# Performance work log

Hardware: AMD Instinct MI355X
Metric: run time of the kernel (lower is better)

The kernel has to match this reference:

```python
import jax, jax.numpy as jnp
import numpy as np

NUM_EXPERTS = 8
INTERM_D = 64  # hardcoded in DynamicConv


def setup_inputs() -> dict:
    key = jax.random.key(0)
    k1, k2, k3, k4 = jax.random.split(key, 4)
    B, C, H, W = 32, 256, 56, 56
    O, K = 256, 3
    x = jax.random.normal(k1, (B, C, H, W), dtype=jnp.float32)
    proj_w = jax.random.normal(k2, (INTERM_D, C), dtype=jnp.float32) * (1.0 / np.sqrt(C))
    proj_b = jax.random.normal(k3, (INTERM_D,), dtype=jnp.float32) * 0.01
    expert_w = jax.random.normal(k4, (NUM_EXPERTS, O, C, K, K), dtype=jnp.float32) * (1.0 / np.sqrt(C * K * K))
    return {"x": x, "proj_w": proj_w, "proj_b": proj_b, "expert_w": expert_w}


def reference(x, proj_w, proj_b, expert_w):
    B, C, H, W = x.shape
    E, O, Cg, K, _ = expert_w.shape
    # --- routing path ---
    pooled = x.mean(axis=(2, 3))                       # [B, C] adaptive_avg_pool2d(.,1)
    rt = pooled @ proj_w.T + proj_b                    # [B, 64]
    r = jax.nn.sigmoid(rt).reshape(B, E, INTERM_D // E).mean(axis=-1)  # avg_pool1d -> [B, E]
    # --- per-sample expert-mixed conv weights ---
    w = jnp.einsum("be,eoikl->boikl", r, expert_w)     # [B, O, C, K, K]
    # --- batched conv via grouped conv (groups = B) ---
    xr = x.reshape(1, B * C, H, W)
    wr = w.reshape(B * O, Cg, K, K)
    out = jax.lax.conv_general_dilated(
        xr, wr,
        window_strides=(1, 1),
        padding=((1, 1), (1, 1)),
        dimension_numbers=("NCHW", "OIHW", "NCHW"),
        feature_group_count=B,
    )                                                   # [1, B*O, H, W]
    return out.reshape(B, O, H, W)
```

## Files before the change

### kernel.cpp

```cpp
#include <hip/hip_runtime.h>
#include <math.h>

typedef unsigned short u16;
typedef __attribute__((ext_vector_type(8))) short    bf16x8;
typedef __attribute__((ext_vector_type(8))) unsigned short u16x8;
typedef __attribute__((ext_vector_type(4))) float    f32x4;

#define NB   32
#define NC   256
#define NO   256
#define NH   56
#define NW   56
#define NP   3136
#define NE   8
#define NID  64
#define HP   58
#define WP   64

#define WMIX_OFF   0
#define XPT_OFF    37748736
#define POOL_OFF   98566144
#define RBUF_OFF   98598912

__device__ __forceinline__ u16 f2bf(float f) {
    unsigned u = __float_as_uint(f);
    unsigned r = (u + 0x7FFFu + ((u >> 16) & 1u)) >> 16;
    return (u16)r;
}

__device__ __forceinline__ void gl_lds16(const void* g, void* l) {
    __builtin_amdgcn_global_load_lds(
        (const __attribute__((address_space(1))) unsigned int*)g,
        (__attribute__((address_space(3))) unsigned int*)l, 16, 0, 0);
}

#define VMCNT0_FENCE() { asm volatile("s_waitcnt vmcnt(0)" ::: "memory"); \
                         __builtin_amdgcn_sched_barrier(0); }

__global__ __launch_bounds__(256) void zero_k(float* __restrict__ pooled,
                                              u16* __restrict__ xpadT) {
    int b = blockIdx.x, t = threadIdx.x;
    pooled[b * 256 + t] = 0.0f;
    u16x8 z = {0, 0, 0, 0, 0, 0, 0, 0};
    u16* r0 = xpadT + ((size_t)(b * HP + 0)) * WP * NC;
    u16* r1 = xpadT + ((size_t)(b * HP + 57)) * WP * NC;
    #pragma unroll
    for (int i = 0; i < 8; ++i) {
        *(u16x8*)&r0[(i * 256 + t) * 8] = z;
        *(u16x8*)&r1[(i * 256 + t) * 8] = z;
    }
}

__global__ __launch_bounds__(256) void transpose_pool_k(const float* __restrict__ x,
                                                        u16* __restrict__ xpadT,
                                                        float* __restrict__ pooled) {
    __shared__ u16 tile[64 * 256];
    int b = blockIdx.x / 56;
    int h = blockIdx.x % 56;
    int t = threadIdx.x;

    int w4 = t & 15, c_sub = t >> 4;
    if (w4 < 14) {
        const float* xp = x + ((size_t)b * NC + c_sub) * NP + (size_t)h * NW + w4 * 4;
        #pragma unroll
        for (int it = 0; it < 16; ++it) {
            int c = it * 16 + c_sub;
            f32x4 v = *(const f32x4*)(xp + (size_t)it * 16 * NP);
            int key = w4;
            int base = ((c >> 3) ^ key) * 8 + (c & 7);
            #pragma unroll
            for (int i = 0; i < 4; ++i)
                tile[(w4 * 4 + i) * 256 + base] = f2bf(v[i]);
        }
    }
    __syncthreads();

    {
        int c8 = t & 31, whi = t >> 5;
        u16* orow = xpadT + ((size_t)(b * HP + h + 1)) * WP * NC;
        #pragma unroll
        for (int j = 0; j < 8; ++j) {
            int wp = whi * 8 + j;
            u16x8 v = {0, 0, 0, 0, 0, 0, 0, 0};
            if (wp >= 1 && wp <= 56) {
                int w = wp - 1;
                v = *(const u16x8*)&tile[w * 256 + ((c8 ^ (w >> 2)) * 8)];
            }
            *(u16x8*)&orow[wp * NC + c8 * 8] = v;
        }
    }

    {
        int c = t;
        int s = c >> 3, sub = c & 7;
        float sum = 0.0f;
        #pragma unroll
        for (int w = 0; w < 56; ++w) {
            u16 u = tile[w * 256 + ((s ^ (w >> 2)) * 8) + sub];
            sum += __uint_as_float(((unsigned)u) << 16);
        }
        atomicAdd(&pooled[b * 256 + c], sum);
    }
}

__global__ __launch_bounds__(64) void routing(const float* __restrict__ pooled,
                                              const float* __restrict__ proj_w,
                                              const float* __restrict__ proj_b,
                                              float* __restrict__ r) {
    __shared__ float ps[256];
    __shared__ float sg[64];
    int b = blockIdx.x, j = threadIdx.x;
    for (int i = j; i < 256; i += 64) ps[i] = pooled[b * NC + i] * (1.0f / 3136.0f);
    __syncthreads();
    float acc = proj_b[j];
    for (int c = 0; c < 256; ++c) acc += ps[c] * proj_w[j * NC + c];
    sg[j] = 1.0f / (1.0f + expf(-acc));
    __syncthreads();
    if (j < NE) {
        float s = 0.0f;
        #pragma unroll
        for (int q = 0; q < 8; ++q) s += sg[j * 8 + q];
        r[b * NE + j] = s * 0.125f;
    }
}

__global__ __launch_bounds__(256) void mix_w(const float* __restrict__ expert_w,
                                             const float* __restrict__ r,
                                             u16* __restrict__ wmix) {
    __shared__ float lr[256];
    int o = blockIdx.x, c = threadIdx.x;
    lr[c] = r[c];
    __syncthreads();
    float w[8][9];
    #pragma unroll
    for (int e = 0; e < 8; ++e) {
        const float* p = expert_w + ((size_t)((e * NO + o) * NC + c)) * 9;
        #pragma unroll
        for (int kk = 0; kk < 9; ++kk) w[e][kk] = p[kk];
    }
    for (int b = 0; b < NB; ++b) {
        float acc[9] = {0, 0, 0, 0, 0, 0, 0, 0, 0};
        #pragma unroll
        for (int e = 0; e < 8; ++e) {
            float rv = lr[b * 8 + e];
            #pragma unroll
            for (int kk = 0; kk < 9; ++kk) acc[kk] += rv * w[e][kk];
        }
        #pragma unroll
        for (int kk = 0; kk < 9; ++kk)
            wmix[((size_t)((b * 9 + kk) * NO + o)) * NC + c] = f2bf(acc[kk]);
    }
}

__global__ __launch_bounds__(256, 2) void conv_k(const u16* __restrict__ wmix,
                                                 const u16* __restrict__ xpadT,
                                                 float* __restrict__ out) {
    __shared__ u16 Bs[256 * 64];
    __shared__ u16 As[2 * 128 * 64];
    char* Bsc = (char*)Bs;
    char* Asc = (char*)As;

    int tid  = threadIdx.x;
    int lane = tid & 63, wid = tid >> 6;
    int ln = lane & 15, hi = lane >> 4;

    int bid = blockIdx.x;
    int logical = (bid & 7) * 224 + (bid >> 3);
    int b   = logical / 56;
    int rem = logical % 56;
    int mt  = rem / 28, nt = rem % 28;
    int obase = mt * 128;
    int h0 = nt * 2;
    int p0 = nt * 112;

    const u16* apane = wmix + (size_t)b * 9 * 65536 + (size_t)obase * 256;
    const u16* xbase = xpadT + ((size_t)(b * HP + h0)) * WP * NC;

    int t3 = tid >> 3, t7 = tid & 7;
    int bstg_src = t3 * 256 + ((t7 ^ (t3 & 7)) * 8);
    int bstg_dst = tid * 16;
    #define STAGE_B(C0) {                                                   \
        _Pragma("unroll")                                                   \
        for (int i = 0; i < 8; ++i)                                         \
            gl_lds16(xbase + (C0) + bstg_src + i * 8192,                    \
                     Bsc + bstg_dst + i * 4096);                            \
    }

    int l3 = lane >> 3, l7 = lane & 7;
    int astg_src = (wid * 32 + l3) * 256 + ((l7 ^ (l3 & 7)) * 8);
    int astg_dst = wid * 4096 + lane * 16;
    #define STAGE_A(KK, C0, BUF) {                                          \
        _Pragma("unroll")                                                   \
        for (int i = 0; i < 4; ++i)                                         \
            gl_lds16(apane + (KK) * 65536 + (C0) + astg_src + i * 2048,     \
                     Asc + (BUF) * 16384 + astg_dst + i * 1024);            \
    }

    f32x4 acc[2][7];
    #pragma unroll
    for (int mi = 0; mi < 2; ++mi)
        #pragma unroll
        for (int ni = 0; ni < 7; ++ni) acc[mi][ni] = (f32x4){0.f, 0.f, 0.f, 0.f};

    int rwbase[7];
    #pragma unroll
    for (int ni = 0; ni < 7; ++ni) {
        int p  = ni * 16 + ln;
        int hr = (p >= 56) ? 1 : 0;
        int wv = p - hr * 56;
        rwbase[ni] = hr * 64 + wv + 1;
    }
    int aoff[2][2];
    #pragma unroll
    for (int mi = 0; mi < 2; ++mi)
        #pragma unroll
        for (int ks = 0; ks < 2; ++ks)
            aoff[mi][ks] = wid * 4096 + (mi * 16 + ln) * 128 +
                           (((ks * 4 + hi) ^ (ln & 7)) << 4);

    STAGE_B(0)
    STAGE_A(0, 0, 0)
    __syncthreads();

    for (int c0 = 0; c0 < 256; c0 += 64) {
        int cc = (c0 >> 6) & 1;
        #pragma unroll
        for (int kk = 0; kk < 9; ++kk) {
            int cur = (cc + kk) & 1;
            if (kk < 8) {
                STAGE_A(kk + 1, c0, cur ^ 1)
            } else if (c0 < 192) {
                STAGE_A(0, c0 + 64, cur ^ 1)
            }
            const int dh = kk / 3, kw = kk % 3;
            const int abase = cur * 16384;
            #pragma unroll
            for (int ks = 0; ks < 2; ++ks) {
                bf16x8 a0 = *(const bf16x8*)(Asc + abase + aoff[0][ks]);
                bf16x8 a1 = *(const bf16x8*)(Asc + abase + aoff[1][ks]);
                #pragma unroll
                for (int ni = 0; ni < 7; ++ni) {
                    int rw   = rwbase[ni] + dh * 64 + kw - 1;
                    int boff = rw * 128 + ((((ks << 2) + hi) ^ (rw & 7)) << 4);
                    bf16x8 bv = *(const bf16x8*)(Bsc + boff);
                    acc[0][ni] = __builtin_amdgcn_mfma_f32_16x16x32_bf16(a0, bv, acc[0][ni], 0, 0, 0);
                    acc[1][ni] = __builtin_amdgcn_mfma_f32_16x16x32_bf16(a1, bv, acc[1][ni], 0, 0, 0);
                }
            }
            VMCNT0_FENCE()
        }
        if (c0 < 192) {
            __syncthreads();
            STAGE_B(c0 + 64)
            __syncthreads();
        }
    }
    #undef STAGE_A
    #undef STAGE_B

    float* op = out + ((size_t)(b * NO + obase + wid * 32)) * NP + p0;
    #pragma unroll
    for (int mi = 0; mi < 2; ++mi)
        #pragma unroll
        for (int ni = 0; ni < 7; ++ni) {
            f32x4 v = acc[mi][ni];
            int col = ni * 16 + ln;
            #pragma unroll
            for (int rg = 0; rg < 4; ++rg) {
                int row = mi * 16 + hi * 4 + rg;
                op[(size_t)row * NP + col] = v[rg];
            }
        }
}

extern "C" void kernel_launch(void* const* d_in, const int* in_sizes, int n_in,
                              void* d_out, int out_size, void* d_ws, size_t ws_size,
                              hipStream_t stream) {
    (void)in_sizes; (void)n_in; (void)out_size; (void)ws_size;
    const float* x        = (const float*)d_in[0];
    const float* proj_w   = (const float*)d_in[1];
    const float* proj_b   = (const float*)d_in[2];
    const float* expert_w = (const float*)d_in[3];
    float* out = (float*)d_out;
    char*  ws  = (char*)d_ws;

    u16*   wmix   = (u16*)(ws + WMIX_OFF);
    u16*   xpadT  = (u16*)(ws + XPT_OFF);
    float* pooled = (float*)(ws + POOL_OFF);
    float* rbuf   = (float*)(ws + RBUF_OFF);

    zero_k<<<dim3(32), dim3(256), 0, stream>>>(pooled, xpadT);
    transpose_pool_k<<<dim3(32 * 56), dim3(256), 0, stream>>>(x, xpadT, pooled);
    routing<<<dim3(32), dim3(64), 0, stream>>>(pooled, proj_w, proj_b, rbuf);
    mix_w<<<dim3(256), dim3(256), 0, stream>>>(expert_w, rbuf, wmix);
    conv_k<<<dim3(32 * 56), dim3(256), 0, stream>>>(wmix, xpadT, out);
}
```

Before: 209.6 us.

## Cover all output channels per block and load weight fragments directly into registers

```diff
diff --git a/kernel.cpp b/kernel.cpp
--- a/kernel.cpp
+++ b/kernel.cpp
@@ -34,9 +34,6 @@
         (__attribute__((address_space(3))) unsigned int*)l, 16, 0, 0);
 }
 
-#define VMCNT0_FENCE() { asm volatile("s_waitcnt vmcnt(0)" ::: "memory"); \
-                         __builtin_amdgcn_sched_barrier(0); }
-
 __global__ __launch_bounds__(256) void zero_k(float* __restrict__ pooled,
                                               u16* __restrict__ xpadT) {
     int b = blockIdx.x, t = threadIdx.x;
@@ -156,25 +153,23 @@
                                                  const u16* __restrict__ xpadT,
                                                  float* __restrict__ out) {
     __shared__ u16 Bs[256 * 64];
-    __shared__ u16 As[2 * 128 * 64];
     char* Bsc = (char*)Bs;
-    char* Asc = (char*)As;
 
     int tid  = threadIdx.x;
     int lane = tid & 63, wid = tid >> 6;
     int ln = lane & 15, hi = lane >> 4;
 
     int bid = blockIdx.x;
-    int logical = (bid & 7) * 224 + (bid >> 3);
-    int b   = logical / 56;
-    int rem = logical % 56;
-    int mt  = rem / 28, nt = rem % 28;
-    int obase = mt * 128;
+    int logical = (bid & 7) * 112 + (bid >> 3);
+    int b  = logical / 28;
+    int nt = logical % 28;
     int h0 = nt * 2;
     int p0 = nt * 112;
 
-    const u16* apane = wmix + (size_t)b * 9 * 65536 + (size_t)obase * 256;
+    const u16* apane = wmix + (size_t)b * 9 * 65536;
     const u16* xbase = xpadT + ((size_t)(b * HP + h0)) * WP * NC;
+
+    const u16* alane = apane + (size_t)(wid * 64 + ln) * 256 + hi * 8;
 
     int t3 = tid >> 3, t7 = tid & 7;
     int bstg_src = t3 * 256 + ((t7 ^ (t3 & 7)) * 8);
@@ -186,19 +181,19 @@
                      Bsc + bstg_dst + i * 4096);                            \
     }
 
-    int l3 = lane >> 3, l7 = lane & 7;
-    int astg_src = (wid * 32 + l3) * 256 + ((l7 ^ (l3 & 7)) * 8);
-    int astg_dst = wid * 4096 + lane * 16;
-    #define STAGE_A(KK, C0, BUF) {                                          \
+    bf16x8 abuf0[8], abuf1[8];
+    #define ISSUE_A(KK, C0, ABUF) {                                         \
+        const u16* ap_ = alane + (KK) * 65536 + (C0);                       \
         _Pragma("unroll")                                                   \
-        for (int i = 0; i < 4; ++i)                                         \
-            gl_lds16(apane + (KK) * 65536 + (C0) + astg_src + i * 2048,     \
-                     Asc + (BUF) * 16384 + astg_dst + i * 1024);            \
-    }
-
-    f32x4 acc[2][7];
-    #pragma unroll
-    for (int mi = 0; mi < 2; ++mi)
+        for (int mi = 0; mi < 4; ++mi) {                                    \
+            ABUF[mi * 2 + 0] = *(const bf16x8*)(ap_ + mi * 4096);           \
+            ABUF[mi * 2 + 1] = *(const bf16x8*)(ap_ + mi * 4096 + 32);      \
+        }                                                                   \
+    }
+
+    f32x4 acc[4][7];
+    #pragma unroll
+    for (int mi = 0; mi < 4; ++mi)
         #pragma unroll
         for (int ni = 0; ni < 7; ++ni) acc[mi][ni] = (f32x4){0.f, 0.f, 0.f, 0.f};
 
@@ -210,57 +205,52 @@
         int wv = p - hr * 56;
         rwbase[ni] = hr * 64 + wv + 1;
     }
-    int aoff[2][2];
-    #pragma unroll
-    for (int mi = 0; mi < 2; ++mi)
-        #pragma unroll
-        for (int ks = 0; ks < 2; ++ks)
-            aoff[mi][ks] = wid * 4096 + (mi * 16 + ln) * 128 +
-                           (((ks * 4 + hi) ^ (ln & 7)) << 4);
+
+    #define TAP_COMPUTE(KK, ABUF) {                                         \
+        const int dh = (KK) / 3, kw = (KK) % 3;                             \
+        _Pragma("unroll")                                                   \
+        for (int ks = 0; ks < 2; ++ks) {                                    \
+            _Pragma("unroll")                                               \
+            for (int ni = 0; ni < 7; ++ni) {                                \
+                int rw   = rwbase[ni] + dh * 64 + kw - 1;                   \
+                int boff = rw * 128 + ((((ks << 2) + hi) ^ (rw & 7)) << 4); \
+                bf16x8 bv = *(const bf16x8*)(Bsc + boff);                   \
+                acc[0][ni] = __builtin_amdgcn_mfma_f32_16x16x32_bf16(ABUF[0 * 2 + ks], bv, acc[0][ni], 0, 0, 0); \
+                acc[1][ni] = __builtin_amdgcn_mfma_f32_16x16x32_bf16(ABUF[1 * 2 + ks], bv, acc[1][ni], 0, 0, 0); \
+                acc[2][ni] = __builtin_amdgcn_mfma_f32_16x16x32_bf16(ABUF[2 * 2 + ks], bv, acc[2][ni], 0, 0, 0); \
+                acc[3][ni] = __builtin_amdgcn_mfma_f32_16x16x32_bf16(ABUF[3 * 2 + ks], bv, acc[3][ni], 0, 0, 0); \
+            }                                                               \
+        }                                                                   \
+    }
 
     STAGE_B(0)
-    STAGE_A(0, 0, 0)
+    ISSUE_A(0, 0, abuf0)
     __syncthreads();
 
     for (int c0 = 0; c0 < 256; c0 += 64) {
-        int cc = (c0 >> 6) & 1;
-        #pragma unroll
-        for (int kk = 0; kk < 9; ++kk) {
-            int cur = (cc + kk) & 1;
-            if (kk < 8) {
-                STAGE_A(kk + 1, c0, cur ^ 1)
-            } else if (c0 < 192) {
-                STAGE_A(0, c0 + 64, cur ^ 1)
-            }
-            const int dh = kk / 3, kw = kk % 3;
-            const int abase = cur * 16384;
-            #pragma unroll
-            for (int ks = 0; ks < 2; ++ks) {
-                bf16x8 a0 = *(const bf16x8*)(Asc + abase + aoff[0][ks]);
-                bf16x8 a1 = *(const bf16x8*)(Asc + abase + aoff[1][ks]);
-                #pragma unroll
-                for (int ni = 0; ni < 7; ++ni) {
-                    int rw   = rwbase[ni] + dh * 64 + kw - 1;
-                    int boff = rw * 128 + ((((ks << 2) + hi) ^ (rw & 7)) << 4);
-                    bf16x8 bv = *(const bf16x8*)(Bsc + boff);
-                    acc[0][ni] = __builtin_amdgcn_mfma_f32_16x16x32_bf16(a0, bv, acc[0][ni], 0, 0, 0);
-                    acc[1][ni] = __builtin_amdgcn_mfma_f32_16x16x32_bf16(a1, bv, acc[1][ni], 0, 0, 0);
-                }
-            }
-            VMCNT0_FENCE()
-        }
+        ISSUE_A(1, c0, abuf1)  TAP_COMPUTE(0, abuf0)
+        ISSUE_A(2, c0, abuf0)  TAP_COMPUTE(1, abuf1)
+        ISSUE_A(3, c0, abuf1)  TAP_COMPUTE(2, abuf0)
+        ISSUE_A(4, c0, abuf0)  TAP_COMPUTE(3, abuf1)
+        ISSUE_A(5, c0, abuf1)  TAP_COMPUTE(4, abuf0)
+        ISSUE_A(6, c0, abuf0)  TAP_COMPUTE(5, abuf1)
+        ISSUE_A(7, c0, abuf1)  TAP_COMPUTE(6, abuf0)
+        ISSUE_A(8, c0, abuf0)  TAP_COMPUTE(7, abuf1)
+        TAP_COMPUTE(8, abuf0)
         if (c0 < 192) {
             __syncthreads();
+            ISSUE_A(0, c0 + 64, abuf0)
             STAGE_B(c0 + 64)
             __syncthreads();
         }
     }
-    #undef STAGE_A
+    #undef TAP_COMPUTE
+    #undef ISSUE_A
     #undef STAGE_B
 
-    float* op = out + ((size_t)(b * NO + obase + wid * 32)) * NP + p0;
-    #pragma unroll
-    for (int mi = 0; mi < 2; ++mi)
+    float* op = out + ((size_t)(b * NO + wid * 64)) * NP + p0;
+    #pragma unroll
+    for (int mi = 0; mi < 4; ++mi)
         #pragma unroll
         for (int ni = 0; ni < 7; ++ni) {
             f32x4 v = acc[mi][ni];
@@ -293,5 +283,5 @@
     transpose_pool_k<<<dim3(32 * 56), dim3(256), 0, stream>>>(x, xpadT, pooled);
     routing<<<dim3(32), dim3(64), 0, stream>>>(pooled, proj_w, proj_b, rbuf);
     mix_w<<<dim3(256), dim3(256), 0, stream>>>(expert_w, rbuf, wmix);
-    conv_k<<<dim3(32 * 56), dim3(256), 0, stream>>>(wmix, xpadT, out);
-}
+    conv_k<<<dim3(32 * 28), dim3(256), 0, stream>>>(wmix, xpadT, out);
+}
```

Measured after the change: 272.9 us. 1.3x slower.
